# Performance work log

Hardware: AMD Instinct MI355X
Metric: run time of the kernel (lower is better)

## Reference

```python
import jax, jax.numpy as jnp
import numpy as np

N_NODES = 50000
N_EDGES = 800000
IN_C, HID_C, MID_C = 128, 64, 32


def setup_inputs() -> dict:
    key = jax.random.key(0)
    ks = jax.random.split(key, 9)
    x = jax.random.normal(ks[0], (N_NODES, IN_C), dtype=jnp.float32)
    edge_index = jax.random.randint(ks[1], (2, N_EDGES), 0, N_NODES, dtype=jnp.int32)
    def glorot(k, fan_in, fan_out):
        s = jnp.sqrt(6.0 / (fan_in + fan_out))
        return jax.random.uniform(k, (fan_in, fan_out), jnp.float32, -s, s)
    return {
        "x": x,
        "edge_index": edge_index,
        "W1": glorot(ks[2], IN_C, HID_C), "b1": jnp.zeros((HID_C,), jnp.float32),
        "W2": glorot(ks[3], HID_C, MID_C), "b2": jnp.zeros((MID_C,), jnp.float32),
        "W3": glorot(ks[4], MID_C, 1), "b3": jnp.zeros((1,), jnp.float32),
    }


def _gcn_layer(x, src, dst, edge_norm, W, b):
    # linear transform, then normalized gather-scale-scatter aggregation
    h = x @ W                                   # [N, F_out]
    msg = h[src] * edge_norm[:, None]           # [E+N, F_out]
    out = jax.ops.segment_sum(msg, dst, num_segments=x.shape[0])
    return out + b


def reference(x, edge_index, W1, b1, W2, b2, W3, b3):
    n = x.shape[0]
    loop = jnp.arange(n, dtype=edge_index.dtype)
    src = jnp.concatenate([edge_index[0], loop])   # A + I (self loops)
    dst = jnp.concatenate([edge_index[1], loop])
    # symmetric degree normalization D^{-1/2} (A+I) D^{-1/2}
    deg = jax.ops.segment_sum(jnp.ones_like(dst, dtype=x.dtype), dst, num_segments=n)
    dinv = jnp.where(deg > 0, jax.lax.rsqrt(deg), 0.0)
    edge_norm = dinv[src] * dinv[dst]              # [E+N]

    h = jax.nn.relu(_gcn_layer(x, src, dst, edge_norm, W1, b1))
    h = jax.nn.relu(_gcn_layer(h, src, dst, edge_norm, W2, b2))
    h = _gcn_layer(h, src, dst, edge_norm, W3, b3)
    return jnp.squeeze(h, axis=-1)                 # [N]
```

## Files before the change

kernel.cpp:

```cpp
#include <hip/hip_runtime.h>
#include <hip/hip_fp16.h>


#define IN_C 128
#define NPB_SHIFT 8
#define BCAP 5120

static __device__ __forceinline__ float2 up2(unsigned u) {
    __half2 h = *reinterpret_cast<__half2*>(&u);
    return __half22float2(h);
}
static __device__ __forceinline__ unsigned pk2(float a, float b) {
    __half2 h = __floats2half2_rn(a, b);
    return *reinterpret_cast<unsigned*>(&h);
}
static __device__ __forceinline__ int wave_incl_scan(int v, int lane) {
#pragma unroll
    for (int off = 1; off < 64; off <<= 1) {
        const int u = __shfl_up(v, off);
        if (lane >= off) v += u;
    }
    return v;
}

#define ACC8(v) { float2 f_; \
    f_ = up2((v).x); a[0] += f_.x; a[1] += f_.y; \
    f_ = up2((v).y); a[2] += f_.x; a[3] += f_.y; \
    f_ = up2((v).z); a[4] += f_.x; a[5] += f_.y; \
    f_ = up2((v).w); a[6] += f_.x; a[7] += f_.y; }


__global__ void zero256_kernel(int* __restrict__ p) { p[threadIdx.x] = 0; }


__global__ __launch_bounds__(256) void partition_kernel(
    const int* __restrict__ src, const int* __restrict__ dst,
    int* __restrict__ bucketcur, unsigned* __restrict__ tmp, int n_edges, int nb) {
    constexpr int EPT = 8;
    __shared__ int hist[256];
    __shared__ int excl[256];
    __shared__ int rankc[256];
    __shared__ int gbase[256];
    __shared__ int wsum[4];
    __shared__ unsigned sorted[256 * EPT];

    const int t = threadIdx.x;
    const int lane = t & 63;
    const int w = t >> 6;
    const int e0 = blockIdx.x * 256 * EPT;
    hist[t] = 0;
    rankc[t] = 0;
    __syncthreads();

    int d[EPT], s[EPT];
#pragma unroll
    for (int i = 0; i < EPT; ++i) {
        const int e = e0 + t + i * 256;
        if (e < n_edges) {
            d[i] = dst[e];
            s[i] = src[e];
            atomicAdd(&hist[d[i] >> NPB_SHIFT], 1);
        } else {
            d[i] = -1;
        }
    }
    __syncthreads();

    const int hv = hist[t];
    const int inc = wave_incl_scan(hv, lane);
    if (lane == 63) wsum[w] = inc;
    __syncthreads();
    int base = 0;
#pragma unroll
    for (int i = 0; i < 4; ++i)
        if (i < w) base += wsum[i];
    excl[t] = base + inc - hv;
    if (t < nb && hv > 0) gbase[t] = t * BCAP + atomicAdd(&bucketcur[t], hv);
    __syncthreads();

#pragma unroll
    for (int i = 0; i < EPT; ++i) {
        if (d[i] >= 0) {
            const int b = d[i] >> NPB_SHIFT;
            const int r = atomicAdd(&rankc[b], 1);
            sorted[excl[b] + r] = ((unsigned)d[i] << 16) | (unsigned)s[i];
        }
    }
    __syncthreads();

    const int m = min(256 * EPT, n_edges - e0);
    for (int i = t; i < m; i += 256) {
        const unsigned pk = sorted[i];
        const int b = (int)(pk >> 24);
        tmp[gbase[b] + (i - excl[b])] = pk;
    }
}


__global__ __launch_bounds__(256) void local_fill_kernel(
    const unsigned* __restrict__ tmp, const int* __restrict__ bucketcur,
    int* __restrict__ row_start, int* __restrict__ deg, float* __restrict__ dinv,
    int* __restrict__ esrc, int n_nodes) {
    __shared__ int histl[256];
    __shared__ int cur[256];
    __shared__ int wsum[4];
    __shared__ unsigned eb[BCAP];
    const int b = blockIdx.x;
    const int base = b * BCAP;
    const int t = threadIdx.x;
    const int lane = t & 63;
    const int w = t >> 6;
    const int m = min(bucketcur[b], BCAP);
    histl[t] = 0;
    __syncthreads();

    for (int i = t; i < m; i += 256) {
        const unsigned p = tmp[base + i];
        eb[i] = p;
        atomicAdd(&histl[(p >> 16) & 255u], 1);
    }
    __syncthreads();

    const int hv = histl[t];
    const int inc = wave_incl_scan(hv, lane);
    if (lane == 63) wsum[w] = inc;
    __syncthreads();
    int wb = 0;
#pragma unroll
    for (int i = 0; i < 4; ++i)
        if (i < w) wb += wsum[i];
    const int rs = base + wb + inc - hv;
    const int node = (b << NPB_SHIFT) + t;
    if (node < n_nodes) {
        row_start[node] = rs;
        deg[node] = hv;
        dinv[node] = rsqrtf((float)hv + 1.0f);
    }
    cur[t] = rs;
    __syncthreads();

    for (int i = t; i < m; i += 256) {
        const unsigned p = eb[i];
        const int pos = atomicAdd(&cur[(p >> 16) & 255u], 1);
        esrc[pos] = (int)(p & 0xFFFFu);
    }
}


__global__ __launch_bounds__(256) void gemm1_kernel(
    const float* __restrict__ x, const float* __restrict__ W,
    const float* __restrict__ dinv, __half* __restrict__ g1h, int n_nodes) {
    constexpr int KDIM = 128, COUT = 64;
    __shared__ float Wl[KDIM * COUT];
    const int tid = threadIdx.x;
#pragma unroll
    for (int i = 0; i < KDIM * COUT / 1024; ++i) {
        const int idx = (i * 256 + tid) * 4;
        *(float4*)&Wl[idx] = *(const float4*)&W[idx];
    }
    __syncthreads();

    const int tx = tid % 16;
    const int ty = tid / 16;
    const int c0 = tx * 4;
    const int n0 = blockIdx.x * 64 + ty * 4;

    const float4* xr[4];
#pragma unroll
    for (int nn = 0; nn < 4; ++nn) {
        const int node = n0 + nn;
        xr[nn] = (const float4*)(x + (size_t)(node < n_nodes ? node : 0) * KDIM);
    }

    float acc[4][4] = {};
#pragma unroll 4
    for (int k4 = 0; k4 < KDIM / 4; ++k4) {
        float4 xv[4], wv[4];
#pragma unroll
        for (int nn = 0; nn < 4; ++nn) xv[nn] = xr[nn][k4];
#pragma unroll
        for (int kk = 0; kk < 4; ++kk)
            wv[kk] = *(const float4*)&Wl[(k4 * 4 + kk) * COUT + c0];
#pragma unroll
        for (int nn = 0; nn < 4; ++nn) {
            const float xs0 = xv[nn].x, xs1 = xv[nn].y, xs2 = xv[nn].z, xs3 = xv[nn].w;
            acc[nn][0] = fmaf(xs0, wv[0].x, fmaf(xs1, wv[1].x, fmaf(xs2, wv[2].x, fmaf(xs3, wv[3].x, acc[nn][0]))));
            acc[nn][1] = fmaf(xs0, wv[0].y, fmaf(xs1, wv[1].y, fmaf(xs2, wv[2].y, fmaf(xs3, wv[3].y, acc[nn][1]))));
            acc[nn][2] = fmaf(xs0, wv[0].z, fmaf(xs1, wv[1].z, fmaf(xs2, wv[2].z, fmaf(xs3, wv[3].z, acc[nn][2]))));
            acc[nn][3] = fmaf(xs0, wv[0].w, fmaf(xs1, wv[1].w, fmaf(xs2, wv[2].w, fmaf(xs3, wv[3].w, acc[nn][3]))));
        }
    }

#pragma unroll
    for (int nn = 0; nn < 4; ++nn) {
        const int node = n0 + nn;
        if (node < n_nodes) {
            const float dv = dinv[node];
            uint2 pk;
            pk.x = pk2(acc[nn][0] * dv, acc[nn][1] * dv);
            pk.y = pk2(acc[nn][2] * dv, acc[nn][3] * dv);
            *(uint2*)&g1h[(size_t)node * COUT + c0] = pk;
        }
    }
}


__global__ __launch_bounds__(256) void agg64_kernel(
    const int* __restrict__ row_start, const int* __restrict__ deg,
    const int* __restrict__ esrc, const __half* __restrict__ g1h,
    const float* __restrict__ dinv, const float* __restrict__ b1,
    __half* __restrict__ z1h, int n) {
    const int t = threadIdx.x;
    const int lane = t & 63;
    const int c4 = lane & 7;
    const int node = blockIdx.x * 32 + (t >> 6) * 8 + (lane >> 3);
    if (node >= n) return;
    const uint4* __restrict__ tab = (const uint4*)g1h;
    const int beg = row_start[node];
    const int dg = deg[node];

    float a[8] = {};
    int i = 0;
    if (dg >= 8) {
        int s0 = esrc[beg], s1 = esrc[beg + 1], s2 = esrc[beg + 2], s3 = esrc[beg + 3];
        for (; i + 8 <= dg; i += 4) {
            const int t0 = esrc[beg + i + 4], t1 = esrc[beg + i + 5],
                      t2 = esrc[beg + i + 6], t3 = esrc[beg + i + 7];
            const uint4 v0 = tab[(size_t)s0 * 8 + c4];
            const uint4 v1 = tab[(size_t)s1 * 8 + c4];
            const uint4 v2 = tab[(size_t)s2 * 8 + c4];
            const uint4 v3 = tab[(size_t)s3 * 8 + c4];
            ACC8(v0); ACC8(v1); ACC8(v2); ACC8(v3);
            s0 = t0; s1 = t1; s2 = t2; s3 = t3;
        }
        const uint4 v0 = tab[(size_t)s0 * 8 + c4];
        const uint4 v1 = tab[(size_t)s1 * 8 + c4];
        const uint4 v2 = tab[(size_t)s2 * 8 + c4];
        const uint4 v3 = tab[(size_t)s3 * 8 + c4];
        ACC8(v0); ACC8(v1); ACC8(v2); ACC8(v3);
        i += 4;
    }
    for (; i + 4 <= dg; i += 4) {
        const int s0 = esrc[beg + i], s1 = esrc[beg + i + 1],
                  s2 = esrc[beg + i + 2], s3 = esrc[beg + i + 3];
        const uint4 v0 = tab[(size_t)s0 * 8 + c4];
        const uint4 v1 = tab[(size_t)s1 * 8 + c4];
        const uint4 v2 = tab[(size_t)s2 * 8 + c4];
        const uint4 v3 = tab[(size_t)s3 * 8 + c4];
        ACC8(v0); ACC8(v1); ACC8(v2); ACC8(v3);
    }
    for (; i < dg; ++i) {
        const uint4 v = tab[(size_t)esrc[beg + i] * 8 + c4];
        ACC8(v);
    }

    const float dv = dinv[node];
    const uint4 sv = tab[(size_t)node * 8 + c4];
    const float2 f0 = up2(sv.x), f1 = up2(sv.y), f2 = up2(sv.z), f3 = up2(sv.w);
    const float4 bb0 = ((const float4*)b1)[c4 * 2];
    const float4 bb1 = ((const float4*)b1)[c4 * 2 + 1];
    uint4 o;
    o.x = pk2(fmaxf(dv * (a[0] + f0.x) + bb0.x, 0.0f),
              fmaxf(dv * (a[1] + f0.y) + bb0.y, 0.0f));
    o.y = pk2(fmaxf(dv * (a[2] + f1.x) + bb0.z, 0.0f),
              fmaxf(dv * (a[3] + f1.y) + bb0.w, 0.0f));
    o.z = pk2(fmaxf(dv * (a[4] + f2.x) + bb1.x, 0.0f),
              fmaxf(dv * (a[5] + f2.y) + bb1.y, 0.0f));
    o.w = pk2(fmaxf(dv * (a[6] + f3.x) + bb1.z, 0.0f),
              fmaxf(dv * (a[7] + f3.y) + bb1.w, 0.0f));
    ((uint4*)z1h)[(size_t)node * 8 + c4] = o;
}


__global__ __launch_bounds__(256) void gemm2_kernel(
    const __half* __restrict__ z1h, const float* __restrict__ W2,
    const float* __restrict__ dinv, __half* __restrict__ g2h, int n_nodes) {
    __shared__ float Wl[64 * 32];
    const int tid = threadIdx.x;
    {
        const float4* Ws = (const float4*)W2;
        float4* Wd = (float4*)Wl;
        Wd[tid] = Ws[tid];
        Wd[tid + 256] = Ws[tid + 256];
    }
    __syncthreads();

    const int tx = tid & 7;
    const int ty = tid >> 3;
    const int c0 = tx * 4;
    const int n0 = blockIdx.x * 128 + ty * 4;

    const uint2* xr[4];
#pragma unroll
    for (int nn = 0; nn < 4; ++nn) {
        const int node = n0 + nn;
        xr[nn] = (const uint2*)(z1h + (size_t)(node < n_nodes ? node : 0) * 64);
    }

    float acc[4][4] = {};
#pragma unroll 4
    for (int k4 = 0; k4 < 16; ++k4) {
        float4 wv[4];
#pragma unroll
        for (int kk = 0; kk < 4; ++kk)
            wv[kk] = *(const float4*)&Wl[(k4 * 4 + kk) * 32 + c0];
#pragma unroll
        for (int nn = 0; nn < 4; ++nn) {
            const uint2 xv = xr[nn][k4];
            const float2 xlo = up2(xv.x), xhi = up2(xv.y);
            acc[nn][0] = fmaf(xlo.x, wv[0].x, fmaf(xlo.y, wv[1].x, fmaf(xhi.x, wv[2].x, fmaf(xhi.y, wv[3].x, acc[nn][0]))));
            acc[nn][1] = fmaf(xlo.x, wv[0].y, fmaf(xlo.y, wv[1].y, fmaf(xhi.x, wv[2].y, fmaf(xhi.y, wv[3].y, acc[nn][1]))));
            acc[nn][2] = fmaf(xlo.x, wv[0].z, fmaf(xlo.y, wv[1].z, fmaf(xhi.x, wv[2].z, fmaf(xhi.y, wv[3].z, acc[nn][2]))));
            acc[nn][3] = fmaf(xlo.x, wv[0].w, fmaf(xlo.y, wv[1].w, fmaf(xhi.x, wv[2].w, fmaf(xhi.y, wv[3].w, acc[nn][3]))));
        }
    }

#pragma unroll
    for (int nn = 0; nn < 4; ++nn) {
        const int node = n0 + nn;
        if (node < n_nodes) {
            const float dv = dinv[node];
            uint2 o;
            o.x = pk2(acc[nn][0] * dv, acc[nn][1] * dv);
            o.y = pk2(acc[nn][2] * dv, acc[nn][3] * dv);
            *(uint2*)&g2h[(size_t)node * 32 + c0] = o;
        }
    }
}


__global__ __launch_bounds__(256) void agg32_gemm3_kernel(
    const int* __restrict__ row_start, const int* __restrict__ deg,
    const int* __restrict__ esrc, const __half* __restrict__ g2h,
    const float* __restrict__ dinv, const float* __restrict__ b2,
    const float* __restrict__ W3, float* __restrict__ g3, int n) {
    const int t = threadIdx.x;
    const int lane = t & 63;
    const int c2 = lane & 3;
    const int node = blockIdx.x * 64 + (t >> 6) * 16 + (lane >> 2);
    if (node >= n) return;
    const uint4* __restrict__ tab = (const uint4*)g2h;
    const int beg = row_start[node];
    const int dg = deg[node];

    float a[8] = {};
    int i = 0;
    if (dg >= 8) {
        int s0 = esrc[beg], s1 = esrc[beg + 1], s2 = esrc[beg + 2], s3 = esrc[beg + 3];
        for (; i + 8 <= dg; i += 4) {
            const int t0 = esrc[beg + i + 4], t1 = esrc[beg + i + 5],
                      t2 = esrc[beg + i + 6], t3 = esrc[beg + i + 7];
            const uint4 v0 = tab[(size_t)s0 * 4 + c2];
            const uint4 v1 = tab[(size_t)s1 * 4 + c2];
            const uint4 v2 = tab[(size_t)s2 * 4 + c2];
            const uint4 v3 = tab[(size_t)s3 * 4 + c2];
            ACC8(v0); ACC8(v1); ACC8(v2); ACC8(v3);
            s0 = t0; s1 = t1; s2 = t2; s3 = t3;
        }
        const uint4 v0 = tab[(size_t)s0 * 4 + c2];
        const uint4 v1 = tab[(size_t)s1 * 4 + c2];
        const uint4 v2 = tab[(size_t)s2 * 4 + c2];
        const uint4 v3 = tab[(size_t)s3 * 4 + c2];
        ACC8(v0); ACC8(v1); ACC8(v2); ACC8(v3);
        i += 4;
    }
    for (; i + 4 <= dg; i += 4) {
        const int s0 = esrc[beg + i], s1 = esrc[beg + i + 1],
                  s2 = esrc[beg + i + 2], s3 = esrc[beg + i + 3];
        const uint4 v0 = tab[(size_t)s0 * 4 + c2];
        const uint4 v1 = tab[(size_t)s1 * 4 + c2];
        const uint4 v2 = tab[(size_t)s2 * 4 + c2];
        const uint4 v3 = tab[(size_t)s3 * 4 + c2];
        ACC8(v0); ACC8(v1); ACC8(v2); ACC8(v3);
    }
    for (; i < dg; ++i) {
        const uint4 v = tab[(size_t)esrc[beg + i] * 4 + c2];
        ACC8(v);
    }

    const float dv = dinv[node];
    const uint4 sv = tab[(size_t)node * 4 + c2];
    const float2 f0 = up2(sv.x), f1 = up2(sv.y), f2 = up2(sv.z), f3 = up2(sv.w);
    const float4 bb0 = ((const float4*)b2)[c2 * 2];
    const float4 bb1 = ((const float4*)b2)[c2 * 2 + 1];
    const float4 w0 = ((const float4*)W3)[c2 * 2];
    const float4 w1 = ((const float4*)W3)[c2 * 2 + 1];
    float p = 0.0f;
    p = fmaf(fmaxf(dv * (a[0] + f0.x) + bb0.x, 0.0f), w0.x, p);
    p = fmaf(fmaxf(dv * (a[1] + f0.y) + bb0.y, 0.0f), w0.y, p);
    p = fmaf(fmaxf(dv * (a[2] + f1.x) + bb0.z, 0.0f), w0.z, p);
    p = fmaf(fmaxf(dv * (a[3] + f1.y) + bb0.w, 0.0f), w0.w, p);
    p = fmaf(fmaxf(dv * (a[4] + f2.x) + bb1.x, 0.0f), w1.x, p);
    p = fmaf(fmaxf(dv * (a[5] + f2.y) + bb1.y, 0.0f), w1.y, p);
    p = fmaf(fmaxf(dv * (a[6] + f3.x) + bb1.z, 0.0f), w1.z, p);
    p = fmaf(fmaxf(dv * (a[7] + f3.y) + bb1.w, 0.0f), w1.w, p);
    p += __shfl_xor(p, 1);
    p += __shfl_xor(p, 2);
    if (c2 == 0) g3[node] = p * dv;
}


__global__ __launch_bounds__(256) void agg_kernel1(
    const int* __restrict__ row_start, const int* __restrict__ deg,
    const int* __restrict__ esrc, const float* __restrict__ g,
    const float* __restrict__ dinv, const float* __restrict__ b3,
    float* __restrict__ out, int n) {
    const int node = blockIdx.x * 32 + (threadIdx.x >> 3);
    if (node >= n) return;
    const int l = threadIdx.x & 7;
    const int beg = row_start[node], end = beg + deg[node];
    float acc = 0.0f;
    for (int e = beg + l; e < end; e += 8)
        acc += g[esrc[e]];
    acc += __shfl_xor(acc, 1);
    acc += __shfl_xor(acc, 2);
    acc += __shfl_xor(acc, 4);
    if (l == 0) out[node] = dinv[node] * (acc + g[node]) + b3[0];
}


extern "C" void kernel_launch(void* const* d_in, const int* in_sizes, int n_in,
                              void* d_out, int out_size, void* d_ws, size_t ws_size,
                              hipStream_t stream) {
    const float* x  = (const float*)d_in[0];
    const int*   ei = (const int*)d_in[1];
    const float* W1 = (const float*)d_in[2];
    const float* b1 = (const float*)d_in[3];
    const float* W2 = (const float*)d_in[4];
    const float* b2 = (const float*)d_in[5];
    const float* W3 = (const float*)d_in[6];
    const float* b3 = (const float*)d_in[7];
    float* out = (float*)d_out;

    const int n_nodes = in_sizes[0] / IN_C;
    const int n_edges = in_sizes[1] / 2;
    const int* src = ei;
    const int* dst = ei + n_edges;
    const int nbuckets = (n_nodes + (1 << NPB_SHIFT) - 1) >> NPB_SHIFT;

    auto align_up = [](size_t v) { return (v + 255) & ~(size_t)255; };
    char* p = (char*)d_ws;
    int*      bucketcur = (int*)p;     p += align_up(256 * 4);
    int*      row_start = (int*)p;     p += align_up((size_t)n_nodes * 4);
    int*      deg       = (int*)p;     p += align_up((size_t)n_nodes * 4);
    float*    dinv      = (float*)p;   p += align_up((size_t)n_nodes * 4);
    int*      esrc      = (int*)p;     p += align_up((size_t)nbuckets * BCAP * 4);
    __half*   g1h       = (__half*)p;  p += align_up((size_t)n_nodes * 64 * 2);
    __half*   z1h       = (__half*)p;  p += align_up((size_t)n_nodes * 64 * 2);
    char* up = p;
    unsigned* tmp       = (unsigned*)up;
    __half*   g2h       = (__half*)up;
    float*    g3        = (float*)(up + align_up((size_t)n_nodes * 32 * 2));
    (void)ws_size; (void)n_in; (void)out_size;

    zero256_kernel<<<1, 256, 0, stream>>>(bucketcur);
    partition_kernel<<<(n_edges + 2047) / 2048, 256, 0, stream>>>(src, dst, bucketcur, tmp, n_edges, nbuckets);
    local_fill_kernel<<<nbuckets, 256, 0, stream>>>(tmp, bucketcur, row_start, deg, dinv, esrc, n_nodes);

    gemm1_kernel<<<(n_nodes + 63) / 64, 256, 0, stream>>>(x, W1, dinv, g1h, n_nodes);
    agg64_kernel<<<(n_nodes + 31) / 32, 256, 0, stream>>>(row_start, deg, esrc, g1h, dinv, b1, z1h, n_nodes);
    gemm2_kernel<<<(n_nodes + 127) / 128, 256, 0, stream>>>(z1h, W2, dinv, g2h, n_nodes);

    agg32_gemm3_kernel<<<(n_nodes + 63) / 64, 256, 0, stream>>>(row_start, deg, esrc, g2h, dinv, b2, W3, g3, n_nodes);

    agg_kernel1<<<(n_nodes + 31) / 32, 256, 0, stream>>>(row_start, deg, esrc, g3, dinv, b3, out, n_nodes);
}
```

Before: 95.22 us.

## Degree-sort nodes within buckets and shrink edge source indices to 16-bit

local_fill_kernel now bins each bucket's nodes by degree (capped at 63) and writes a per-bucket permutation. The three aggregation kernels walk nodes in that order, so lanes in a wave handle nodes of similar degree, which should cut loop divergence and idle lanes. The edge source array is also stored as unsigned short instead of int, halving index traffic. In exchange, each aggregation kernel does an extra indirect load through perm, its output writes become scattered within each bucket, and node ids are limited to below 65536.

```diff
diff --git a/kernel.cpp b/kernel.cpp
--- a/kernel.cpp
+++ b/kernel.cpp
@@ -100,10 +100,13 @@
 __global__ __launch_bounds__(256) void local_fill_kernel(
     const unsigned* __restrict__ tmp, const int* __restrict__ bucketcur,
     int* __restrict__ row_start, int* __restrict__ deg, float* __restrict__ dinv,
-    int* __restrict__ esrc, int n_nodes) {
+    int* __restrict__ perm, unsigned short* __restrict__ esrc, int n_nodes) {
     __shared__ int histl[256];
     __shared__ int cur[256];
     __shared__ int wsum[4];
+    __shared__ int dhist[64];
+    __shared__ int dexcl[64];
+    __shared__ int dcur[64];
     __shared__ unsigned eb[BCAP];
     const int b = blockIdx.x;
     const int base = b * BCAP;
@@ -112,6 +115,7 @@
     const int w = t >> 6;
     const int m = min(bucketcur[b], BCAP);
     histl[t] = 0;
+    if (t < 64) { dhist[t] = 0; dcur[t] = 0; }
     __syncthreads();
 
     for (int i = t; i < m; i += 256) {
@@ -131,18 +135,30 @@
         if (i < w) wb += wsum[i];
     const int rs = base + wb + inc - hv;
     const int node = (b << NPB_SHIFT) + t;
+    const int bin = min(hv, 63);
     if (node < n_nodes) {
         row_start[node] = rs;
         deg[node] = hv;
         dinv[node] = rsqrtf((float)hv + 1.0f);
+        atomicAdd(&dhist[bin], 1);
     }
     cur[t] = rs;
     __syncthreads();
+
+    if (t < 64) {
+        const int v = dhist[t];
+        dexcl[t] = wave_incl_scan(v, t) - v;
+    }
+    __syncthreads();
+    if (node < n_nodes) {
+        const int r = atomicAdd(&dcur[bin], 1);
+        perm[(b << NPB_SHIFT) + dexcl[bin] + r] = node;
+    }
 
     for (int i = t; i < m; i += 256) {
         const unsigned p = eb[i];
         const int pos = atomicAdd(&cur[(p >> 16) & 255u], 1);
-        esrc[pos] = (int)(p & 0xFFFFu);
+        esrc[pos] = (unsigned short)(p & 0xFFFFu);
     }
 }
 
@@ -207,14 +223,15 @@
 
 __global__ __launch_bounds__(256) void agg64_kernel(
     const int* __restrict__ row_start, const int* __restrict__ deg,
-    const int* __restrict__ esrc, const __half* __restrict__ g1h,
-    const float* __restrict__ dinv, const float* __restrict__ b1,
-    __half* __restrict__ z1h, int n) {
+    const int* __restrict__ perm, const unsigned short* __restrict__ esrc,
+    const __half* __restrict__ g1h, const float* __restrict__ dinv,
+    const float* __restrict__ b1, __half* __restrict__ z1h, int n) {
     const int t = threadIdx.x;
     const int lane = t & 63;
     const int c4 = lane & 7;
-    const int node = blockIdx.x * 32 + (t >> 6) * 8 + (lane >> 3);
-    if (node >= n) return;
+    const int pos = blockIdx.x * 32 + (t >> 6) * 8 + (lane >> 3);
+    if (pos >= n) return;
+    const int node = perm[pos];
     const uint4* __restrict__ tab = (const uint4*)g1h;
     const int beg = row_start[node];
     const int dg = deg[node];
@@ -331,14 +348,16 @@
 
 __global__ __launch_bounds__(256) void agg32_gemm3_kernel(
     const int* __restrict__ row_start, const int* __restrict__ deg,
-    const int* __restrict__ esrc, const __half* __restrict__ g2h,
-    const float* __restrict__ dinv, const float* __restrict__ b2,
-    const float* __restrict__ W3, float* __restrict__ g3, int n) {
+    const int* __restrict__ perm, const unsigned short* __restrict__ esrc,
+    const __half* __restrict__ g2h, const float* __restrict__ dinv,
+    const float* __restrict__ b2, const float* __restrict__ W3,
+    float* __restrict__ g3, int n) {
     const int t = threadIdx.x;
     const int lane = t & 63;
     const int c2 = lane & 3;
-    const int node = blockIdx.x * 64 + (t >> 6) * 16 + (lane >> 2);
-    if (node >= n) return;
+    const int pos = blockIdx.x * 64 + (t >> 6) * 16 + (lane >> 2);
+    if (pos >= n) return;
+    const int node = perm[pos];
     const uint4* __restrict__ tab = (const uint4*)g2h;
     const int beg = row_start[node];
     const int dg = deg[node];
@@ -402,11 +421,12 @@
 
 __global__ __launch_bounds__(256) void agg_kernel1(
     const int* __restrict__ row_start, const int* __restrict__ deg,
-    const int* __restrict__ esrc, const float* __restrict__ g,
-    const float* __restrict__ dinv, const float* __restrict__ b3,
-    float* __restrict__ out, int n) {
-    const int node = blockIdx.x * 32 + (threadIdx.x >> 3);
-    if (node >= n) return;
+    const int* __restrict__ perm, const unsigned short* __restrict__ esrc,
+    const float* __restrict__ g, const float* __restrict__ dinv,
+    const float* __restrict__ b3, float* __restrict__ out, int n) {
+    const int pos = blockIdx.x * 32 + (threadIdx.x >> 3);
+    if (pos >= n) return;
+    const int node = perm[pos];
     const int l = threadIdx.x & 7;
     const int beg = row_start[node], end = beg + deg[node];
     float acc = 0.0f;
@@ -440,28 +460,29 @@
 
     auto align_up = [](size_t v) { return (v + 255) & ~(size_t)255; };
     char* p = (char*)d_ws;
-    int*      bucketcur = (int*)p;     p += align_up(256 * 4);
-    int*      row_start = (int*)p;     p += align_up((size_t)n_nodes * 4);
-    int*      deg       = (int*)p;     p += align_up((size_t)n_nodes * 4);
-    float*    dinv      = (float*)p;   p += align_up((size_t)n_nodes * 4);
-    int*      esrc      = (int*)p;     p += align_up((size_t)nbuckets * BCAP * 4);
-    __half*   g1h       = (__half*)p;  p += align_up((size_t)n_nodes * 64 * 2);
-    __half*   z1h       = (__half*)p;  p += align_up((size_t)n_nodes * 64 * 2);
+    int*            bucketcur = (int*)p;            p += align_up(256 * 4);
+    int*            row_start = (int*)p;            p += align_up((size_t)n_nodes * 4);
+    int*            deg       = (int*)p;            p += align_up((size_t)n_nodes * 4);
+    float*          dinv      = (float*)p;          p += align_up((size_t)n_nodes * 4);
+    int*            perm      = (int*)p;            p += align_up((size_t)n_nodes * 4);
+    unsigned short* esrc      = (unsigned short*)p; p += align_up((size_t)nbuckets * BCAP * 2);
+    __half*         g1h       = (__half*)p;         p += align_up((size_t)n_nodes * 64 * 2);
+    __half*         z1h       = (__half*)p;         p += align_up((size_t)n_nodes * 64 * 2);
     char* up = p;
-    unsigned* tmp       = (unsigned*)up;
-    __half*   g2h       = (__half*)up;
-    float*    g3        = (float*)(up + align_up((size_t)n_nodes * 32 * 2));
+    unsigned*       tmp       = (unsigned*)up;
+    __half*         g2h       = (__half*)up;
+    float*          g3        = (float*)(up + align_up((size_t)n_nodes * 32 * 2));
     (void)ws_size; (void)n_in; (void)out_size;
 
     zero256_kernel<<<1, 256, 0, stream>>>(bucketcur);
     partition_kernel<<<(n_edges + 2047) / 2048, 256, 0, stream>>>(src, dst, bucketcur, tmp, n_edges, nbuckets);
-    local_fill_kernel<<<nbuckets, 256, 0, stream>>>(tmp, bucketcur, row_start, deg, dinv, esrc, n_nodes);
+    local_fill_kernel<<<nbuckets, 256, 0, stream>>>(tmp, bucketcur, row_start, deg, dinv, perm, esrc, n_nodes);
 
     gemm1_kernel<<<(n_nodes + 63) / 64, 256, 0, stream>>>(x, W1, dinv, g1h, n_nodes);
-    agg64_kernel<<<(n_nodes + 31) / 32, 256, 0, stream>>>(row_start, deg, esrc, g1h, dinv, b1, z1h, n_nodes);
+    agg64_kernel<<<(n_nodes + 31) / 32, 256, 0, stream>>>(row_start, deg, perm, esrc, g1h, dinv, b1, z1h, n_nodes);
     gemm2_kernel<<<(n_nodes + 127) / 128, 256, 0, stream>>>(z1h, W2, dinv, g2h, n_nodes);
 
-    agg32_gemm3_kernel<<<(n_nodes + 63) / 64, 256, 0, stream>>>(row_start, deg, esrc, g2h, dinv, b2, W3, g3, n_nodes);
-
-    agg_kernel1<<<(n_nodes + 31) / 32, 256, 0, stream>>>(row_start, deg, esrc, g3, dinv, b3, out, n_nodes);
-}
+    agg32_gemm3_kernel<<<(n_nodes + 63) / 64, 256, 0, stream>>>(row_start, deg, perm, esrc, g2h, dinv, b2, W3, g3, n_nodes);
+
+    agg_kernel1<<<(n_nodes + 31) / 32, 256, 0, stream>>>(row_start, deg, perm, esrc, g3, dinv, b3, out, n_nodes);
+}
```

Result: slower. 100.5 us (+5.6%).
